# Kernel optimization log

Hardware: AMD Instinct MI355X
Metric: run time of the kernel (lower is better)

The kernel has to match this reference:

```python
import jax, jax.numpy as jnp
import numpy as np

N_NODES = 100000
N_EDGES = 800000
IN_C, HID, OUT_C = 128, 64, 1


def setup_inputs() -> dict:
    key = jax.random.key(0)
    ks = jax.random.split(key, 12)
    x = jax.random.normal(ks[0], (N_NODES, IN_C), dtype=jnp.float32)
    edge_index = jax.random.randint(ks[1], (2, N_EDGES), 0, N_NODES, dtype=jnp.int64)

    def glorot(k, fan_in, fan_out):
        s = jnp.sqrt(6.0 / (fan_in + fan_out)).astype(jnp.float32)
        return jax.random.uniform(k, (fan_in, fan_out), jnp.float32, -s, s)

    return {
        "x": x,
        "edge_index": edge_index,
        "W1": glorot(ks[2], IN_C, 4 * HID), "b1": jnp.zeros((4 * HID,), jnp.float32),
        "W2": glorot(ks[3], 4 * HID, 2 * HID), "b2": jnp.zeros((2 * HID,), jnp.float32),
        "W3": glorot(ks[4], 2 * HID, HID), "b3": jnp.zeros((HID,), jnp.float32),
        "Wl": glorot(ks[5], HID, OUT_C), "bl": jnp.zeros((OUT_C,), jnp.float32),
    }


def _gcn_conv(x, W, b, src, dst, dinv, n_nodes):
    # PyG GCNConv: D^{-1/2} (A + I) D^{-1/2} X W + b
    xt = x @ W                                   # [N, F_out]
    coef = (dinv[src] * dinv[dst])[:, None]      # [E, 1] symmetric norm
    agg = jax.ops.segment_sum(xt[src] * coef, dst, num_segments=n_nodes)
    agg = agg + (dinv * dinv)[:, None] * xt      # self-loop term (norm = 1/deg)
    return agg + b


def reference(x, edge_index, W1, b1, W2, b2, W3, b3, Wl, bl):
    n = x.shape[0]
    src, dst = edge_index[0], edge_index[1]
    # degree with self loops (edge weight 1), as in gcn_norm(add_self_loops=True)
    deg = jax.ops.segment_sum(jnp.ones_like(dst, dtype=x.dtype), dst, num_segments=n) + 1.0
    dinv = jax.lax.rsqrt(deg)

    h = jax.nn.relu(_gcn_conv(x, W1, b1, src, dst, dinv, n))
    # dropout(p=0.5) is identity at inference (eval mode)
    h = jax.nn.relu(_gcn_conv(h, W2, b2, src, dst, dinv, n))
    h = jax.nn.relu(_gcn_conv(h, W3, b3, src, dst, dinv, n))
    return h @ Wl + bl
```

## Files before the change

kernel.cpp:

```cpp
#include <hip/hip_runtime.h>
#include <hip/hip_bf16.h>
#include <stdint.h>


typedef __attribute__((ext_vector_type(8))) short bf16x8;
typedef __attribute__((ext_vector_type(16))) float f32x16;

__device__ __forceinline__ float bf_lo(uint32_t u) {
    union { uint32_t i; float f; } v; v.i = u << 16; return v.f;
}
__device__ __forceinline__ float bf_hi(uint32_t u) {
    union { uint32_t i; float f; } v; v.i = u & 0xffff0000u; return v.f;
}
__device__ __forceinline__ float bf_s(uint16_t h) {
    union { uint32_t i; float f; } v; v.i = ((uint32_t)h) << 16; return v.f;
}
__device__ __forceinline__ uint16_t f2bf(float f) {
    union { float f; uint32_t i; } v; v.f = f;
    uint32_t r = v.i + 0x7fffu + ((v.i >> 16) & 1u);
    return (uint16_t)(r >> 16);
}
__device__ __forceinline__ uint32_t packbf(float a, float b) {
    return (uint32_t)f2bf(a) | ((uint32_t)f2bf(b) << 16);
}

__global__ __launch_bounds__(256) void hist_kernel(const int* __restrict__ dst,
                                                   int* __restrict__ cnt, int E) {
    int e = blockIdx.x * 256 + threadIdx.x;
    if (e < E) atomicAdd(&cnt[dst[e]], 1);
}

__global__ __launch_bounds__(256) void dinv_kernel(const int* __restrict__ cnt,
                                                   float* __restrict__ dinv, int N) {
    int i = blockIdx.x * 256 + threadIdx.x;
    if (i < N) dinv[i] = rsqrtf((float)cnt[i] + 1.0f);
}

__global__ __launch_bounds__(256) void scan_blk(const int* __restrict__ cnt,
                                                int* __restrict__ row_ptr,
                                                int* __restrict__ bsum, int N) {
    int b = blockIdx.x, t = threadIdx.x;
    int base = b * 1024 + t * 4;
    int v0 = 0, v1 = 0, v2 = 0, v3 = 0;
    if (base + 3 < N) {
        int4 q = *(const int4*)(cnt + base);
        v0 = q.x; v1 = q.y; v2 = q.z; v3 = q.w;
    } else if (base < N) {
        v0 = cnt[base];
        if (base + 1 < N) v1 = cnt[base + 1];
        if (base + 2 < N) v2 = cnt[base + 2];
    }
    int tsum = v0 + v1 + v2 + v3;
    __shared__ int ps[256];
    ps[t] = tsum;
    __syncthreads();
    for (int off = 1; off < 256; off <<= 1) {
        int x = (t >= off) ? ps[t - off] : 0;
        __syncthreads();
        ps[t] += x;
        __syncthreads();
    }
    int ex = (t == 0) ? 0 : ps[t - 1];
    if (t == 255) bsum[b] = ps[255];
    if (base + 3 < N) {
        int4 w; w.x = ex; w.y = ex + v0; w.z = ex + v0 + v1; w.w = ex + v0 + v1 + v2;
        *(int4*)(row_ptr + base) = w;
    } else if (base < N) {
        row_ptr[base] = ex;
        if (base + 1 < N) row_ptr[base + 1] = ex + v0;
        if (base + 2 < N) row_ptr[base + 2] = ex + v0 + v1;
    }
}

__global__ __launch_bounds__(128) void scan_tops(int* __restrict__ bsum, int NB) {
    __shared__ int ps[128];
    int t = threadIdx.x;
    int v = (t < NB) ? bsum[t] : 0;
    ps[t] = v;
    __syncthreads();
    for (int off = 1; off < 128; off <<= 1) {
        int x = (t >= off) ? ps[t - off] : 0;
        __syncthreads();
        ps[t] += x;
        __syncthreads();
    }
    if (t < NB) bsum[t] = (t == 0) ? 0 : ps[t - 1];
}

__global__ __launch_bounds__(256) void scan_add(int* __restrict__ row_ptr,
                                                const int* __restrict__ bsum,
                                                int N, int E) {
    int b = blockIdx.x, t = threadIdx.x;
    int base = b * 1024 + t * 4;
    int off = bsum[b];
    if (base + 3 < N) {
        int4 q = *(int4*)(row_ptr + base);
        q.x += off; q.y += off; q.z += off; q.w += off;
        *(int4*)(row_ptr + base) = q;
    } else {
        for (int i = 0; i < 4; ++i)
            if (base + i < N) row_ptr[base + i] += off;
    }
    if (b == 0 && t == 0) row_ptr[N] = E;
}

__global__ __launch_bounds__(256) void fill_kernel(const int* __restrict__ src,
                                                   const int* __restrict__ dst,
                                                   const int* __restrict__ row_ptr,
                                                   int* __restrict__ cnt,
                                                   int* __restrict__ csr_src, int E) {
    int e = blockIdx.x * 256 + threadIdx.x;
    if (e < E) {
        int d = dst[e];
        int old = atomicSub(&cnt[d], 1);
        csr_src[row_ptr[d + 1] - old] = src[e];
    }
}

template <int K, int M>
__device__ __forceinline__ void wprep_one(const float* __restrict__ W,
                                          uint16_t* __restrict__ Wt, int j) {
    int m = j / K, k = j % K;
    Wt[j] = f2bf(W[k * M + m]);
}
__global__ __launch_bounds__(256) void wprep(const float* __restrict__ W1,
                                             const float* __restrict__ W2,
                                             const float* __restrict__ W3,
                                             uint16_t* __restrict__ Wt1,
                                             uint16_t* __restrict__ Wt2,
                                             uint16_t* __restrict__ Wt3) {
    int i = blockIdx.x * 256 + threadIdx.x;
    if (i < 32768) {
        wprep_one<128, 256>(W1, Wt1, i);
    } else if (i < 65536) {
        wprep_one<256, 128>(W2, Wt2, i - 32768);
    } else if (i < 73728) {
        wprep_one<128, 64>(W3, Wt3, i - 65536);
    }
}

__global__ __launch_bounds__(256) void scale_cvt(const float* __restrict__ x,
                                                 const float* __restrict__ dinv,
                                                 uint32_t* __restrict__ U, long total) {
    long i = (long)blockIdx.x * 256 + threadIdx.x;
    if (i >= total) return;
    int row = (int)(i >> 6);
    float2 v = ((const float2*)x)[i];
    float d = dinv[row];
    U[i] = packbf(d * v.x, d * v.y);
}

template <bool BIAS_RELU>
__global__ __launch_bounds__(256) void agg128(const uint32_t* __restrict__ U,
                                              const float* __restrict__ dinv,
                                              const int* __restrict__ row_ptr,
                                              const int* __restrict__ csr_src,
                                              const float* __restrict__ bias,
                                              uint32_t* __restrict__ Out, int N) {
    int wave = threadIdx.x >> 6, lane = threadIdx.x & 63;
    int n = blockIdx.x * 4 + wave;
    if (n >= N) return;
    uint32_t u = U[(long)n * 64 + lane];
    float s0 = bf_lo(u), s1 = bf_hi(u);
    int e0 = row_ptr[n], e1 = row_ptr[n + 1];
    for (int e = e0; e < e1; e += 8) {
        int idx[8];
        uint32_t uu[8];
#pragma unroll
        for (int j = 0; j < 8; ++j) {
            int ee = e + j; if (ee > e1 - 1) ee = e1 - 1;
            idx[j] = csr_src[ee];
        }
#pragma unroll
        for (int j = 0; j < 8; ++j) uu[j] = U[(long)idx[j] * 64 + lane];
#pragma unroll
        for (int j = 0; j < 8; ++j) {
            float m = (e + j < e1) ? 1.f : 0.f;
            s0 += m * bf_lo(uu[j]);
            s1 += m * bf_hi(uu[j]);
        }
    }
    float d = dinv[n];
    float r0 = d * s0, r1 = d * s1;
    if constexpr (BIAS_RELU) {
        r0 = fmaxf(r0 + bias[2 * lane], 0.f);
        r1 = fmaxf(r1 + bias[2 * lane + 1], 0.f);
    }
    Out[(long)n * 64 + lane] = packbf(r0, r1);
}

__global__ __launch_bounds__(256) void agg64_head(const uint16_t* __restrict__ U,
                                                  const float* __restrict__ dinv,
                                                  const int* __restrict__ row_ptr,
                                                  const int* __restrict__ csr_src,
                                                  const float* __restrict__ b3,
                                                  const float* __restrict__ Wl,
                                                  const float* __restrict__ bl,
                                                  float* __restrict__ out, int N) {
    int wave = threadIdx.x >> 6, lane = threadIdx.x & 63;
    int n = blockIdx.x * 4 + wave;
    if (n >= N) return;
    float s = bf_s(U[(long)n * 64 + lane]);
    int e0 = row_ptr[n], e1 = row_ptr[n + 1];
    for (int e = e0; e < e1; e += 8) {
        int idx[8];
        uint16_t uu[8];
#pragma unroll
        for (int j = 0; j < 8; ++j) {
            int ee = e + j; if (ee > e1 - 1) ee = e1 - 1;
            idx[j] = csr_src[ee];
        }
#pragma unroll
        for (int j = 0; j < 8; ++j) uu[j] = U[(long)idx[j] * 64 + lane];
#pragma unroll
        for (int j = 0; j < 8; ++j) {
            float m = (e + j < e1) ? 1.f : 0.f;
            s += m * bf_s(uu[j]);
        }
    }
    float h = fmaxf(dinv[n] * s + b3[lane], 0.f);
    float v = h * Wl[lane];
#pragma unroll
    for (int off = 32; off; off >>= 1) v += __shfl_xor(v, off);
    if (lane == 0) out[n] = v + bl[0];
}

template <int K, int M, bool BIAS_RELU, bool SCALE_OUT>
__global__ __launch_bounds__(256, 2) void gemm_mfma(const uint16_t* __restrict__ A,
                                                    const uint16_t* __restrict__ Wt,
                                                    const float* __restrict__ bias,
                                                    const float* __restrict__ dinv,
                                                    uint16_t* __restrict__ Y, int N) {
    constexpr int NT = M / 32;
    constexpr int NK = K / 16;
    constexpr int KC = 64;
    constexpr int SD = KC + 8;
    constexpr int CPR = KC / 8;
    __shared__ short wl[M * SD];

    int t = threadIdx.x;
    int wave = t >> 6, lane = t & 63;
    int l31 = lane & 31, lhi = lane >> 5;
    long row0 = (long)blockIdx.x * 128 + wave * 32;

    bf16x8 afrag[NK];
    {
        long arow = row0 + l31; if (arow > N - 1) arow = N - 1;
        const uint16_t* ap = A + arow * K + lhi * 8;
#pragma unroll
        for (int s = 0; s < NK; ++s)
            afrag[s] = *(const bf16x8*)(ap + s * 16);
    }

    f32x16 acc[NT];
#pragma unroll
    for (int c = 0; c < NT; ++c)
#pragma unroll
        for (int r = 0; r < 16; ++r) acc[c][r] = 0.f;

    int r0 = t / CPR, cc8 = (t % CPR) * 8;
    for (int kc0 = 0; kc0 < K; kc0 += KC) {
#pragma unroll
        for (int r = r0; r < M; r += 256 / CPR)
            *(bf16x8*)(wl + r * SD + cc8) = *(const bf16x8*)(Wt + (long)r * K + kc0 + cc8);
        __syncthreads();
#pragma unroll
        for (int s = 0; s < KC / 16; ++s) {
            const short* bp = wl + l31 * SD + s * 16 + lhi * 8;
#pragma unroll
            for (int c = 0; c < NT; ++c) {
                bf16x8 wfrag = *(const bf16x8*)(bp + c * 32 * SD);
                acc[c] = __builtin_amdgcn_mfma_f32_32x32x16_bf16(
                    wfrag, afrag[kc0 / 16 + s], acc[c], 0, 0, 0);
            }
        }
        __syncthreads();
    }

    long node = row0 + l31;
    bool ok = node < N;
    long nclamp = ok ? node : (N - 1);
    float dn = SCALE_OUT ? dinv[nclamp] : 1.f;
    uint16_t* yp = Y + nclamp * M;
#pragma unroll
    for (int c = 0; c < NT; ++c) {
#pragma unroll
        for (int g = 0; g < 4; ++g) {
            int m0 = c * 32 + g * 8 + 4 * lhi;
            float v[4];
#pragma unroll
            for (int j = 0; j < 4; ++j) {
                float x = acc[c][g * 4 + j];
                if constexpr (BIAS_RELU) x = fmaxf(x + bias[m0 + j], 0.f);
                if constexpr (SCALE_OUT) x *= dn;
                v[j] = x;
            }
            if (ok) {
                uint2 pk; pk.x = packbf(v[0], v[1]); pk.y = packbf(v[2], v[3]);
                *(uint2*)(yp + m0) = pk;
            }
        }
    }
}

extern "C" void kernel_launch(void* const* d_in, const int* in_sizes, int n_in,
                              void* d_out, int out_size, void* d_ws, size_t ws_size,
                              hipStream_t stream) {
    const float* x  = (const float*)d_in[0];
    const int* edge = (const int*)d_in[1];
    const float* W1 = (const float*)d_in[2];
    const float* b1 = (const float*)d_in[3];
    const float* W2 = (const float*)d_in[4];
    const float* b2 = (const float*)d_in[5];
    const float* W3 = (const float*)d_in[6];
    const float* b3 = (const float*)d_in[7];
    const float* Wl = (const float*)d_in[8];
    const float* bl = (const float*)d_in[9];
    float* out = (float*)d_out;

    int N = in_sizes[0] / 128;
    int E = in_sizes[1] / 2;
    const int* src = edge;
    const int* dst = edge + E;

    char* ws = (char*)d_ws;
    size_t off = 0;
    auto alloc = [&](size_t bytes) {
        void* p = ws + off;
        off += (bytes + 255) & ~(size_t)255;
        return p;
    };
    int*      cnt     = (int*)     alloc((size_t)N * 4);
    int*      row_ptr = (int*)     alloc((size_t)(N + 1) * 4);
    float*    dinv    = (float*)   alloc((size_t)N * 4);
    int*      csr_src = (int*)     alloc((size_t)E * 4);
    int*      bsum    = (int*)     alloc(128 * 4);
    uint16_t* Wt1     = (uint16_t*)alloc(256 * 128 * 2);
    uint16_t* Wt2     = (uint16_t*)alloc(128 * 256 * 2);
    uint16_t* Wt3     = (uint16_t*)alloc(64 * 128 * 2);
    uint32_t* B_a     = (uint32_t*)alloc((size_t)N * 64 * 4);
    uint32_t* B_b     = (uint32_t*)alloc((size_t)N * 64 * 4);
    uint32_t* B_c     = (uint32_t*)alloc((size_t)N * 128 * 4);
    (void)ws_size; (void)n_in; (void)out_size;

    int NB = (N + 1023) / 1024;

    hipMemsetAsync(cnt, 0, (size_t)N * 4, stream);
    hist_kernel<<<(E + 255) / 256, 256, 0, stream>>>(dst, cnt, E);
    dinv_kernel<<<(N + 255) / 256, 256, 0, stream>>>(cnt, dinv, N);
    scan_blk<<<NB, 256, 0, stream>>>(cnt, row_ptr, bsum, N);
    scan_tops<<<1, 128, 0, stream>>>(bsum, NB);
    scan_add<<<NB, 256, 0, stream>>>(row_ptr, bsum, N, E);
    fill_kernel<<<(E + 255) / 256, 256, 0, stream>>>(src, dst, row_ptr, cnt, csr_src, E);
    wprep<<<288, 256, 0, stream>>>(W1, W2, W3, Wt1, Wt2, Wt3);

    scale_cvt<<<(int)(((long)N * 64 + 255) / 256), 256, 0, stream>>>(x, dinv, B_a, (long)N * 64);
    agg128<false><<<(N + 3) / 4, 256, 0, stream>>>(B_a, dinv, row_ptr, csr_src, nullptr, B_b, N);
    gemm_mfma<128, 256, true, false><<<(N + 127) / 128, 256, 0, stream>>>(
        (const uint16_t*)B_b, Wt1, b1, nullptr, (uint16_t*)B_c, N);
    gemm_mfma<256, 128, false, true><<<(N + 127) / 128, 256, 0, stream>>>(
        (const uint16_t*)B_c, Wt2, nullptr, dinv, (uint16_t*)B_a, N);
    agg128<true><<<(N + 3) / 4, 256, 0, stream>>>(B_a, dinv, row_ptr, csr_src, b2, B_b, N);
    gemm_mfma<128, 64, false, true><<<(N + 127) / 128, 256, 0, stream>>>(
        (const uint16_t*)B_b, Wt3, nullptr, dinv, (uint16_t*)B_a, N);
    agg64_head<<<(N + 3) / 4, 256, 0, stream>>>(
        (const uint16_t*)B_a, dinv, row_ptr, csr_src, b3, Wl, bl, out, N);
}
```

Baseline: 393.1 us.

## Fuse layer-1 and layer-2 GEMMs keeping the hidden activation in registers

Replaces the two back-to-back MFMA GEMM launches (128->256 with bias+ReLU, then 256->128 with dinv scaling) with a single kernel. The 256-wide intermediate is kept in registers as packed bf16 and rearranged into the second GEMM's operand layout with cross-half-wave shuffles. This drops the N x 256 bf16 intermediate buffer's global write and read, plus one launch. In exchange it raises register pressure (two accumulator sets plus 64 packed values per lane), which can cut occupancy or cause spills.

```diff
diff --git a/kernel.cpp b/kernel.cpp
--- a/kernel.cpp
+++ b/kernel.cpp
@@ -223,6 +223,128 @@
 #pragma unroll
     for (int off = 32; off; off >>= 1) v += __shfl_xor(v, off);
     if (lane == 0) out[n] = v + bl[0];
+}
+
+__global__ __launch_bounds__(256, 2) void gemm_fused12(const uint16_t* __restrict__ A,
+                                                       const uint16_t* __restrict__ Wt1,
+                                                       const float* __restrict__ b1,
+                                                       const uint16_t* __restrict__ Wt2,
+                                                       const float* __restrict__ dinv,
+                                                       uint16_t* __restrict__ Y, int N) {
+    constexpr int SD = 72;
+    __shared__ short wl[256 * SD];
+
+    int t = threadIdx.x;
+    int wave = t >> 6, lane = t & 63;
+    int l31 = lane & 31, lhi = lane >> 5;
+    long row0 = (long)blockIdx.x * 128 + wave * 32;
+
+    bf16x8 afrag[8];
+    {
+        long arow = row0 + l31; if (arow > N - 1) arow = N - 1;
+        const uint16_t* ap = A + arow * 128 + lhi * 8;
+#pragma unroll
+        for (int s = 0; s < 8; ++s)
+            afrag[s] = *(const bf16x8*)(ap + s * 16);
+    }
+
+    f32x16 acc1[8];
+#pragma unroll
+    for (int c = 0; c < 8; ++c)
+#pragma unroll
+        for (int r = 0; r < 16; ++r) acc1[c][r] = 0.f;
+
+    int r0 = t / 8, cc8 = (t % 8) * 8;
+    for (int kc0 = 0; kc0 < 128; kc0 += 64) {
+#pragma unroll
+        for (int r = r0; r < 256; r += 32)
+            *(bf16x8*)(wl + r * SD + cc8) = *(const bf16x8*)(Wt1 + (long)r * 128 + kc0 + cc8);
+        __syncthreads();
+#pragma unroll
+        for (int s = 0; s < 4; ++s) {
+            const short* bp = wl + l31 * SD + s * 16 + lhi * 8;
+#pragma unroll
+            for (int c = 0; c < 8; ++c) {
+                bf16x8 wfrag = *(const bf16x8*)(bp + c * 32 * SD);
+                acc1[c] = __builtin_amdgcn_mfma_f32_32x32x16_bf16(
+                    wfrag, afrag[kc0 / 16 + s], acc1[c], 0, 0, 0);
+            }
+        }
+        __syncthreads();
+    }
+
+    uint32_t pk[32][2];
+#pragma unroll
+    for (int c = 0; c < 8; ++c) {
+#pragma unroll
+        for (int g = 0; g < 4; ++g) {
+            int m0 = c * 32 + g * 8 + 4 * lhi;
+            float4 bv = *(const float4*)(b1 + m0);
+            float v0 = fmaxf(acc1[c][g * 4 + 0] + bv.x, 0.f);
+            float v1 = fmaxf(acc1[c][g * 4 + 1] + bv.y, 0.f);
+            float v2 = fmaxf(acc1[c][g * 4 + 2] + bv.z, 0.f);
+            float v3 = fmaxf(acc1[c][g * 4 + 3] + bv.w, 0.f);
+            pk[c * 4 + g][0] = packbf(v0, v1);
+            pk[c * 4 + g][1] = packbf(v2, v3);
+        }
+    }
+
+    f32x16 acc2[4];
+#pragma unroll
+    for (int c = 0; c < 4; ++c)
+#pragma unroll
+        for (int r = 0; r < 16; ++r) acc2[c][r] = 0.f;
+
+    for (int kc0 = 0; kc0 < 256; kc0 += 64) {
+#pragma unroll
+        for (int r = r0; r < 128; r += 32)
+            *(bf16x8*)(wl + r * SD + cc8) = *(const bf16x8*)(Wt2 + (long)r * 256 + kc0 + cc8);
+        __syncthreads();
+#pragma unroll
+        for (int sl = 0; sl < 4; ++sl) {
+            const int s = kc0 / 16 + sl;
+            uint32_t send0 = lhi ? pk[2 * s][0] : pk[2 * s + 1][0];
+            uint32_t send1 = lhi ? pk[2 * s][1] : pk[2 * s + 1][1];
+            uint32_t rcv0 = __shfl_xor(send0, 32);
+            uint32_t rcv1 = __shfl_xor(send1, 32);
+            uint32_t lc0 = lhi ? pk[2 * s + 1][0] : pk[2 * s][0];
+            uint32_t lc1 = lhi ? pk[2 * s + 1][1] : pk[2 * s][1];
+            union { uint32_t u[4]; bf16x8 v; } hf;
+            hf.u[0] = lhi ? rcv0 : lc0;
+            hf.u[1] = lhi ? rcv1 : lc1;
+            hf.u[2] = lhi ? lc0 : rcv0;
+            hf.u[3] = lhi ? lc1 : rcv1;
+            const short* bp = wl + l31 * SD + sl * 16 + lhi * 8;
+#pragma unroll
+            for (int c = 0; c < 4; ++c) {
+                bf16x8 wfrag = *(const bf16x8*)(bp + c * 32 * SD);
+                acc2[c] = __builtin_amdgcn_mfma_f32_32x32x16_bf16(
+                    wfrag, hf.v, acc2[c], 0, 0, 0);
+            }
+        }
+        __syncthreads();
+    }
+
+    long node = row0 + l31;
+    bool ok = node < N;
+    long nclamp = ok ? node : (N - 1);
+    float dn = dinv[nclamp];
+    uint16_t* yp = Y + nclamp * 128;
+#pragma unroll
+    for (int c = 0; c < 4; ++c) {
+#pragma unroll
+        for (int g = 0; g < 4; ++g) {
+            int m0 = c * 32 + g * 8 + 4 * lhi;
+            float v0 = acc2[c][g * 4 + 0] * dn;
+            float v1 = acc2[c][g * 4 + 1] * dn;
+            float v2 = acc2[c][g * 4 + 2] * dn;
+            float v3 = acc2[c][g * 4 + 3] * dn;
+            if (ok) {
+                uint2 pko; pko.x = packbf(v0, v1); pko.y = packbf(v2, v3);
+                *(uint2*)(yp + m0) = pko;
+            }
+        }
+    }
 }
 
 template <int K, int M, bool BIAS_RELU, bool SCALE_OUT>
@@ -340,7 +462,6 @@
     uint16_t* Wt3     = (uint16_t*)alloc(64 * 128 * 2);
     uint32_t* B_a     = (uint32_t*)alloc((size_t)N * 64 * 4);
     uint32_t* B_b     = (uint32_t*)alloc((size_t)N * 64 * 4);
-    uint32_t* B_c     = (uint32_t*)alloc((size_t)N * 128 * 4);
     (void)ws_size; (void)n_in; (void)out_size;
 
     int NB = (N + 1023) / 1024;
@@ -356,10 +477,8 @@
 
     scale_cvt<<<(int)(((long)N * 64 + 255) / 256), 256, 0, stream>>>(x, dinv, B_a, (long)N * 64);
     agg128<false><<<(N + 3) / 4, 256, 0, stream>>>(B_a, dinv, row_ptr, csr_src, nullptr, B_b, N);
-    gemm_mfma<128, 256, true, false><<<(N + 127) / 128, 256, 0, stream>>>(
-        (const uint16_t*)B_b, Wt1, b1, nullptr, (uint16_t*)B_c, N);
-    gemm_mfma<256, 128, false, true><<<(N + 127) / 128, 256, 0, stream>>>(
-        (const uint16_t*)B_c, Wt2, nullptr, dinv, (uint16_t*)B_a, N);
+    gemm_fused12<<<(N + 127) / 128, 256, 0, stream>>>(
+        (const uint16_t*)B_b, Wt1, b1, Wt2, dinv, (uint16_t*)B_a, N);
     agg128<true><<<(N + 3) / 4, 256, 0, stream>>>(B_a, dinv, row_ptr, csr_src, b2, B_b, N);
     gemm_mfma<128, 64, false, true><<<(N + 127) / 128, 256, 0, stream>>>(
         (const uint16_t*)B_b, Wt3, nullptr, dinv, (uint16_t*)B_a, N);
```

Result: faster. 383.3 us (-2.5%).
